# Performance work log

Hardware: AMD Instinct MI355X
Metric: run time of the kernel (lower is better)

## Reference

```python
import jax, jax.numpy as jnp
import numpy as np

N_NODES = 100000
N_EDGES = 1600000
IN_DIM = 128
HIDDEN = 128
OUT_DIM = 10
N_GRAPHS = 512
N_LAYERS = 3


def setup_inputs() -> dict:
    key = jax.random.key(0)
    ks = jax.random.split(key, 12)
    s_in = 1.0 / np.sqrt(IN_DIM)
    s_h = 1.0 / np.sqrt(HIDDEN)
    return {
        "x": jax.random.normal(ks[0], (N_NODES, IN_DIM), jnp.float32),
        "lin1_w": jax.random.normal(ks[1], (IN_DIM, HIDDEN), jnp.float32) * s_in,
        "lin1_b": jnp.zeros((HIDDEN,), jnp.float32),
        "gcn_w": jax.random.normal(ks[2], (N_LAYERS, HIDDEN, HIDDEN), jnp.float32) * s_h,
        "gcn_b": jnp.zeros((N_LAYERS, HIDDEN), jnp.float32),
        "lin_out_w": jax.random.normal(ks[3], (HIDDEN, HIDDEN), jnp.float32) * s_h,
        "lin_out_b": jnp.zeros((HIDDEN,), jnp.float32),
        "cls_w": jax.random.normal(ks[4], (HIDDEN, OUT_DIM), jnp.float32) * s_h,
        "cls_b": jnp.zeros((OUT_DIM,), jnp.float32),
        "edge_index": jax.random.randint(ks[5], (2, N_EDGES), 0, N_NODES, jnp.int64),
        "batch": jnp.sort(jax.random.randint(ks[6], (N_NODES,), 0, N_GRAPHS, jnp.int64)),
    }


def reference(x, lin1_w, lin1_b, gcn_w, gcn_b, lin_out_w, lin_out_b, cls_w, cls_b, edge_index, batch):
    n = x.shape[0]
    # GCNConv normalization with added self-loops (PyG default)
    row, col = edge_index[0], edge_index[1]
    loop = jnp.arange(n)
    row2 = jnp.concatenate([row, loop])  # source (message origin)
    col2 = jnp.concatenate([col, loop])  # target (aggregation index)
    deg = jax.ops.segment_sum(jnp.ones_like(col2, dtype=x.dtype), col2, num_segments=n)
    dinv = jax.lax.rsqrt(jnp.maximum(deg, 1.0))
    norm = (dinv[row2] * dinv[col2])[:, None]  # [E+N, 1]

    counts = jax.ops.segment_sum(jnp.ones((n,), x.dtype), batch, num_segments=N_GRAPHS)
    counts = jnp.maximum(counts, 1.0)[:, None]

    def readout_mean(h):  # global_mean_pool -> [G, H]
        return jax.ops.segment_sum(h, batch, num_segments=N_GRAPHS) / counts

    # lin1 + elu (dropout = identity in eval mode)
    h = jax.nn.elu(x @ lin1_w + lin1_b)
    reps = readout_mean(h)  # readout_layers[0]; l_sum accumulates layer reps
    for i in range(N_LAYERS):
        hw = h @ gcn_w[i]                       # [N, H]
        msg = norm * hw[row2]                   # gather + scale
        agg = jax.ops.segment_sum(msg, col2, num_segments=n)  # scatter-add
        h = jax.nn.elu(agg + gcn_b[i])          # GCNConv bias then NaOp act
        # pooling op is 'none' (remove_pooling=True): graph unchanged
        reps = reps + readout_mean(h)           # readout_layers[i+1], summed by LaOp 'l_sum'
    g = jax.nn.elu(reps @ lin_out_w + lin_out_b)
    logits = g @ cls_w + cls_b
    return jax.nn.log_softmax(logits, axis=-1)
```

## Files before the change

kernel.cpp:

```cpp
#include <hip/hip_runtime.h>
#include <hip/hip_bf16.h>
#include <math.h>

#define NN 100000
#define NE 1600000
#define HID 128
#define NG 512
#define NB 512
#define RB 196
#define CHUNK 4096
#define NPART ((NE + CHUNK - 1) / CHUNK)
#define GEMM_GRID ((NN + 127) / 128)

typedef unsigned short ushort_t;
typedef __attribute__((ext_vector_type(8))) short bf16x8;
typedef __attribute__((ext_vector_type(8))) unsigned short ushort8_t;
typedef __attribute__((ext_vector_type(4))) float f32x4;

__device__ __forceinline__ ushort_t f2bf(float v) {
    unsigned u = __float_as_uint(v);
    unsigned r = (u + 0x7FFF + ((u >> 16) & 1)) >> 16;
    return (ushort_t)r;
}
__device__ __forceinline__ float bf2f(ushort_t u) {
    return __uint_as_float((unsigned)u << 16);
}


__global__ __launch_bounds__(256) void hist_and_prepw(const int* __restrict__ ecol, int* __restrict__ ghist, int E,
                                                      const float* __restrict__ lin1_w,
                                                      const float* __restrict__ gcn_w,
                                                      ushort_t* __restrict__ wt_hi,
                                                      ushort_t* __restrict__ wt_lo) {
    if (blockIdx.x < 512) {
        __shared__ int lh[NB];
        for (int i = threadIdx.x; i < NB; i += 256) lh[i] = 0;
        __syncthreads();
        for (int e = blockIdx.x * 256 + threadIdx.x; e < E; e += 512 * 256)
            atomicAdd(&lh[ecol[e] / RB], 1);
        __syncthreads();
        for (int i = threadIdx.x; i < NB; i += 256) {
            int c = lh[i];
            if (c) atomicAdd(&ghist[i], c);
        }
    } else {
        int mb = blockIdx.x - 512;
        int m = mb >> 3;
        int chunk = mb & 7;
        const float* W = (m == 0) ? lin1_w : gcn_w + (size_t)(m - 1) * 16384;
        ushort_t* hi = wt_hi + (size_t)m * 16384;
        ushort_t* lo = wt_lo + (size_t)m * 16384;
        for (int i = chunk * 2048 + threadIdx.x; i < (chunk + 1) * 2048; i += 256) {
            int j = i & 7;
            int lane = (i >> 3) & 63;
            int ks = (i >> 9) & 3;
            int ct = (i >> 11) & 7;
            int n = ct * 16 + (lane & 15);
            int k = ks * 32 + (lane >> 4) * 8 + j;
            float v = W[k * 128 + n];
            ushort_t h = f2bf(v);
            hi[i] = h;
            lo[i] = f2bf(v - bf2f(h));
        }
    }
}

__global__ __launch_bounds__(NB) void bucket_scan(const int* __restrict__ ghist, int* __restrict__ brp,
                                                  int* __restrict__ gcur, int* __restrict__ rp,
                                                  const int* __restrict__ batch, float* __restrict__ invcnt) {
    __shared__ int s[NB];
    int t = threadIdx.x;
    int v = ghist[t];
    s[t] = v;
    __syncthreads();
    for (int off = 1; off < NB; off <<= 1) {
        int x = (t >= off) ? s[t - off] : 0;
        __syncthreads();
        s[t] += x;
        __syncthreads();
    }
    int ex = s[t] - v;
    brp[t] = ex;
    gcur[t] = ex;
    if (t == NB - 1) { brp[NB] = s[t]; rp[NN] = s[t]; }

    int lo = 0, hi = NN;
    while (lo < hi) { int m = (lo + hi) >> 1; if (batch[m] < t) lo = m + 1; else hi = m; }
    int s0 = lo;
    lo = 0; hi = NN;
    while (lo < hi) { int m = (lo + hi) >> 1; if (batch[m] < t + 1) lo = m + 1; else hi = m; }
    int c = lo - s0;
    invcnt[t] = 1.0f / (float)(c > 0 ? c : 1);
}

template<bool F32A, int MODE>
__device__ __forceinline__ void gemm_body(int bid, int tid,
                                          const float* __restrict__ A,
                                          const ushort_t* __restrict__ a_bf,
                                          const ushort_t* __restrict__ wt_hi,
                                          const ushort_t* __restrict__ wt_lo,
                                          const float* __restrict__ bias,
                                          const float* __restrict__ dinv,
                                          ushort_t* __restrict__ out0,
                                          int N) {
    const int lane = tid & 63;
    const int wid = tid >> 6;
    const int rowBase = bid * 128 + wid * 32;
    const int rblk = rowBase >> 4;
    const int l15 = lane & 15, lg = lane >> 4;

    f32x4 acc[2][8];
#pragma unroll
    for (int rt = 0; rt < 2; ++rt)
#pragma unroll
        for (int ct = 0; ct < 8; ++ct) acc[rt][ct] = (f32x4){0.f, 0.f, 0.f, 0.f};

#pragma unroll
    for (int ks = 0; ks < 4; ++ks) {
        bf16x8 ahi[2], alo[2];
#pragma unroll
        for (int rt = 0; rt < 2; ++rt) {
            int r = rowBase + rt * 16 + l15;
            if (F32A) {
                float av[8];
                if (r < N) {
                    const float* ap = A + (size_t)r * 128 + ks * 32 + lg * 8;
                    float4 a0 = *(const float4*)(ap);
                    float4 a1 = *(const float4*)(ap + 4);
                    av[0] = a0.x; av[1] = a0.y; av[2] = a0.z; av[3] = a0.w;
                    av[4] = a1.x; av[5] = a1.y; av[6] = a1.z; av[7] = a1.w;
                } else {
#pragma unroll
                    for (int j = 0; j < 8; ++j) av[j] = 0.f;
                }
#pragma unroll
                for (int j = 0; j < 8; ++j) {
                    ushort_t h = f2bf(av[j]);
                    ahi[rt][j] = (short)h;
                    alo[rt][j] = (short)f2bf(av[j] - bf2f(h));
                }
            } else {
                if (r < N) {
                    ahi[rt] = *(const bf16x8*)(a_bf + (size_t)(rblk + rt) * 2048 + (ks * 4 + lg) * 128 + l15 * 8);
                } else {
                    bf16x8 z = {0, 0, 0, 0, 0, 0, 0, 0};
                    ahi[rt] = z;
                }
            }
        }
#pragma unroll
        for (int ct = 0; ct < 8; ++ct) {
            size_t boff = (size_t)(((ct * 4 + ks) * 64 + lane) * 8);
            bf16x8 bhi = *(const bf16x8*)(wt_hi + boff);
            bf16x8 blo = *(const bf16x8*)(wt_lo + boff);
            acc[0][ct] = __builtin_amdgcn_mfma_f32_16x16x32_bf16(ahi[0], bhi, acc[0][ct], 0, 0, 0);
            acc[1][ct] = __builtin_amdgcn_mfma_f32_16x16x32_bf16(ahi[1], bhi, acc[1][ct], 0, 0, 0);
            acc[0][ct] = __builtin_amdgcn_mfma_f32_16x16x32_bf16(ahi[0], blo, acc[0][ct], 0, 0, 0);
            acc[1][ct] = __builtin_amdgcn_mfma_f32_16x16x32_bf16(ahi[1], blo, acc[1][ct], 0, 0, 0);
            if (F32A) {
                acc[0][ct] = __builtin_amdgcn_mfma_f32_16x16x32_bf16(alo[0], bhi, acc[0][ct], 0, 0, 0);
                acc[1][ct] = __builtin_amdgcn_mfma_f32_16x16x32_bf16(alo[1], bhi, acc[1][ct], 0, 0, 0);
            }
        }
    }

#pragma unroll
    for (int rt = 0; rt < 2; ++rt) {
#pragma unroll
        for (int reg = 0; reg < 4; ++reg) {
            int row = rowBase + rt * 16 + lg * 4 + reg;
            if (row >= N) continue;
            if (MODE == 0) {
                int r16 = lg * 4 + reg;
#pragma unroll
                for (int ct = 0; ct < 8; ++ct) {
                    int colc = ct * 16 + l15;
                    float v = acc[rt][ct][reg] + bias[colc];
                    v = v > 0.f ? v : expf(v) - 1.f;
                    out0[(size_t)(rblk + rt) * 2048 + (colc >> 3) * 128 + r16 * 8 + (colc & 7)] = f2bf(v);
                }
            } else {
                float dv = dinv[row];
#pragma unroll
                for (int ct = 0; ct < 8; ++ct) {
                    int colc = ct * 16 + l15;
                    out0[(size_t)row * 128 + colc] = f2bf(acc[rt][ct][reg] * dv);
                }
            }
        }
    }
}

__global__ __launch_bounds__(256) void part_gemm1(const int* __restrict__ erow, const int* __restrict__ ecol,
                                                  int* __restrict__ gcur, unsigned int* __restrict__ pairs, int E,
                                                  const float* __restrict__ x,
                                                  const ushort_t* __restrict__ wt_hi,
                                                  const ushort_t* __restrict__ wt_lo,
                                                  const float* __restrict__ lin1_b,
                                                  ushort_t* __restrict__ h) {
    if (blockIdx.x < NPART) {
        __shared__ int cnt[NB];
        __shared__ int base[NB];
        const int t = threadIdx.x;
        const int e0 = blockIdx.x * CHUNK;
        const int e1 = min(e0 + CHUNK, E);
        for (int i = t; i < NB; i += 256) cnt[i] = 0;
        __syncthreads();
        for (int e = e0 + t; e < e1; e += 256) atomicAdd(&cnt[ecol[e] / RB], 1);
        __syncthreads();
        for (int i = t; i < NB; i += 256) {
            int c = cnt[i];
            base[i] = c ? atomicAdd(&gcur[i], c) : 0;
            cnt[i] = 0;
        }
        __syncthreads();
        for (int e = e0 + t; e < e1; e += 256) {
            int d = ecol[e];
            int b = d / RB;
            int off = atomicAdd(&cnt[b], 1);
            pairs[base[b] + off] = ((unsigned)erow[e] << 8) | (unsigned)(d - b * RB);
        }
    } else {
        gemm_body<true, 0>(blockIdx.x - NPART, threadIdx.x, x, nullptr, wt_hi, wt_lo,
                           lin1_b, nullptr, h, NN);
    }
}

__global__ __launch_bounds__(256) void fill_readout0(const unsigned int* __restrict__ pairs, const int* __restrict__ brp,
                                                     int* __restrict__ rp, float* __restrict__ dinv,
                                                     int* __restrict__ csrc,
                                                     const ushort_t* __restrict__ h,
                                                     const int* __restrict__ batch,
                                                     const float* __restrict__ invcnt,
                                                     float* __restrict__ reps) {
    if (blockIdx.x < NB) {
        __shared__ int cnt[RB];
        __shared__ int cur[RB];
        __shared__ int sc[256];
        const int b = blockIdx.x, t = threadIdx.x;
        const int nbase = b * RB;
        const int s = brp[b], e = brp[b + 1];
        for (int i = t; i < RB; i += 256) cnt[i] = 0;
        __syncthreads();
        for (int i = s + t; i < e; i += 256) atomicAdd(&cnt[pairs[i] & 255u], 1);
        __syncthreads();
        int v = (t < RB) ? cnt[t] : 0;
        sc[t] = v;
        __syncthreads();
        for (int off = 1; off < 256; off <<= 1) {
            int x = (t >= off) ? sc[t - off] : 0;
            __syncthreads();
            sc[t] += x;
            __syncthreads();
        }
        if (t < RB) {
            int ex = s + sc[t] - v;
            int node = nbase + t;
            if (node < NN) {
                rp[node] = ex;
                dinv[node] = rsqrtf((float)v + 1.0f);
            }
            cur[t] = ex;
        }
        __syncthreads();
        for (int i = s + t; i < e; i += 256) {
            unsigned int p = pairs[i];
            int slot = atomicAdd(&cur[p & 255u], 1);
            csrc[slot] = (int)(p >> 8);
        }
    } else {
        int bb = blockIdx.x - NB;
        int g = bb >> 2;
        int part = bb & 3;
        int lo = 0, hi = NN;
        while (lo < hi) { int m = (lo + hi) >> 1; if (batch[m] < g) lo = m + 1; else hi = m; }
        int s = lo;
        lo = 0; hi = NN;
        while (lo < hi) { int m = (lo + hi) >> 1; if (batch[m] < g + 1) lo = m + 1; else hi = m; }
        int e = lo;

        __shared__ float sh[16][136];
        int ns = (int)(threadIdx.x >> 4);
        int L  = (int)(threadIdx.x & 15);
        int c8 = L << 3;
        float acc[8] = {};
        for (int v = s + part + ns * 4; v < e; v += 64) {
            ushort8_t t = *(const ushort8_t*)(h + (size_t)(v >> 4) * 2048 + L * 128 + (v & 15) * 8);
#pragma unroll
            for (int j = 0; j < 8; ++j) acc[j] += bf2f(t[j]);
        }
#pragma unroll
        for (int j = 0; j < 8; ++j) sh[ns][c8 + j] = acc[j];
        __syncthreads();
        if (threadIdx.x < 128) {
            int c = (int)threadIdx.x;
            float sum = 0.f;
#pragma unroll
            for (int k = 0; k < 16; ++k) sum += sh[k][c];
            unsafeAtomicAdd(&reps[(size_t)g * 128 + c], sum * invcnt[g]);
        }
    }
}

__global__ __launch_bounds__(256) void gemm_gcn(const ushort_t* __restrict__ a_bf,
                                                const ushort_t* __restrict__ wt_hi,
                                                const ushort_t* __restrict__ wt_lo,
                                                const float* __restrict__ dinv,
                                                ushort_t* __restrict__ hwb) {
    gemm_body<false, 1>(blockIdx.x, threadIdx.x, nullptr, a_bf, wt_hi, wt_lo,
                        nullptr, dinv, hwb, NN);
}

__global__ __launch_bounds__(256) void gather_agg(const int* __restrict__ rp,
                                                  const int* __restrict__ csrc,
                                                  const float* __restrict__ dinv,
                                                  const ushort_t* __restrict__ hwb,
                                                  const float* __restrict__ bias,
                                                  const int* __restrict__ batch,
                                                  const float* __restrict__ invcnt,
                                                  float* __restrict__ reps,
                                                  ushort_t* __restrict__ h_out) {
    __shared__ float sh[16][136];
    __shared__ int gid[16];
    const int v0 = blockIdx.x * 16;
    const int ns = (int)(threadIdx.x >> 4);
    int v = v0 + ns;
    int L = (int)(threadIdx.x & 15);
    int c8 = L << 3;
    if (threadIdx.x < 16) {
        int bidx = v0 + (int)threadIdx.x;
        if (bidx > NN - 1) bidx = NN - 1;
        gid[threadIdx.x] = batch[bidx];
    }

    float acc[8] = {};
    if (v < NN) {
        int s = rp[v], e = rp[v + 1];
        int i = s;
        for (; i + 16 <= e; i += 16) {
            int u[16];
#pragma unroll
            for (int k = 0; k < 16; ++k) u[k] = csrc[i + k];
            ushort8_t r[16];
#pragma unroll
            for (int k = 0; k < 16; ++k) r[k] = *(const ushort8_t*)(hwb + (size_t)u[k] * 128 + c8);
#pragma unroll
            for (int k = 0; k < 16; ++k)
#pragma unroll
                for (int j = 0; j < 8; ++j) acc[j] += bf2f(r[k][j]);
        }
        for (; i + 8 <= e; i += 8) {
            int u[8];
#pragma unroll
            for (int k = 0; k < 8; ++k) u[k] = csrc[i + k];
            ushort8_t r[8];
#pragma unroll
            for (int k = 0; k < 8; ++k) r[k] = *(const ushort8_t*)(hwb + (size_t)u[k] * 128 + c8);
#pragma unroll
            for (int k = 0; k < 8; ++k)
#pragma unroll
                for (int j = 0; j < 8; ++j) acc[j] += bf2f(r[k][j]);
        }
        for (; i < e; ++i) {
            int u = csrc[i];
            ushort8_t r0 = *(const ushort8_t*)(hwb + (size_t)u * 128 + c8);
#pragma unroll
            for (int j = 0; j < 8; ++j) acc[j] += bf2f(r0[j]);
        }

        float di = dinv[v];
        ushort8_t sv = *(const ushort8_t*)(hwb + (size_t)v * 128 + c8);
        ushort8_t o;
#pragma unroll
        for (int j = 0; j < 8; ++j) {
            float t = di * (acc[j] + bf2f(sv[j])) + bias[c8 + j];
            t = t > 0.f ? t : expf(t) - 1.f;
            acc[j] = t;
            o[j] = f2bf(t);
        }
        *(ushort8_t*)(h_out + (size_t)blockIdx.x * 2048 + L * 128 + ns * 8) = o;
    } else {
#pragma unroll
        for (int j = 0; j < 8; ++j) acc[j] = 0.f;
    }

#pragma unroll
    for (int j = 0; j < 8; ++j) sh[ns][c8 + j] = acc[j];
    __syncthreads();
    if (threadIdx.x < 128) {
        int c = (int)threadIdx.x;
        int nvalid = NN - v0;
        if (nvalid > 16) nvalid = 16;
        float run = sh[0][c];
        int cg = gid[0];
        for (int k = 1; k < nvalid; ++k) {
            int g2 = gid[k];
            if (g2 != cg) {
                unsafeAtomicAdd(&reps[(size_t)cg * 128 + c], run * invcnt[cg]);
                run = 0.f;
                cg = g2;
            }
            run += sh[k][c];
        }
        unsafeAtomicAdd(&reps[(size_t)cg * 128 + c], run * invcnt[cg]);
    }
}

__global__ __launch_bounds__(128) void head_fused(const float* __restrict__ reps,
                                                  const float* __restrict__ wout,
                                                  const float* __restrict__ bout,
                                                  const float* __restrict__ cw,
                                                  const float* __restrict__ cb,
                                                  float* __restrict__ out) {
    __shared__ float rrow[128];
    __shared__ float gg[128];
    __shared__ float lg[10];
    int t = threadIdx.x;
    int g = blockIdx.x;
    rrow[t] = reps[(size_t)g * 128 + t];
    __syncthreads();
    float a = bout[t];
    for (int k = 0; k < 128; ++k) a = fmaf(rrow[k], wout[k * 128 + t], a);
    a = a > 0.f ? a : expf(a) - 1.f;
    gg[t] = a;
    __syncthreads();
    if (t < 10) {
        float s = cb[t];
        for (int k = 0; k < 128; ++k) s = fmaf(gg[k], cw[k * 10 + t], s);
        lg[t] = s;
    }
    __syncthreads();
    if (t == 0) {
        float m = lg[0];
#pragma unroll
        for (int j = 1; j < 10; ++j) m = fmaxf(m, lg[j]);
        float se = 0.f;
#pragma unroll
        for (int j = 0; j < 10; ++j) se += expf(lg[j] - m);
        float L = logf(se);
#pragma unroll
        for (int j = 0; j < 10; ++j) out[(size_t)g * 10 + j] = lg[j] - m - L;
    }
}

extern "C" void kernel_launch(void* const* d_in, const int* in_sizes, int n_in,
                              void* d_out, int out_size, void* d_ws, size_t ws_size,
                              hipStream_t stream) {
    const float* x        = (const float*)d_in[0];
    const float* lin1_w   = (const float*)d_in[1];
    const float* lin1_b   = (const float*)d_in[2];
    const float* gcn_w    = (const float*)d_in[3];
    const float* gcn_b    = (const float*)d_in[4];
    const float* lin_out_w= (const float*)d_in[5];
    const float* lin_out_b= (const float*)d_in[6];
    const float* cls_w    = (const float*)d_in[7];
    const float* cls_b    = (const float*)d_in[8];
    const int*   ei       = (const int*)d_in[9];
    const int*   batch    = (const int*)d_in[10];
    float* out = (float*)d_out;

    const int* erow = ei;
    const int* ecol = ei + NE;

    ushort_t* h     = (ushort_t*)d_ws;
    ushort_t* hwb   = h + (size_t)NN * 128;
    float*    dinv  = (float*)(hwb + (size_t)NN * 128);
    float*    reps  = dinv + NN;
    float*    invcnt= reps + (size_t)NG * 128;
    int*      rp    = (int*)(invcnt + NG);
    int*      csrc  = rp + NN + 1;
    int*      ghist = csrc + NE;
    int*      brp   = ghist + NB;
    int*      gcur  = brp + NB + 1;
    ushort_t* wt_hi = (ushort_t*)(gcur + NB);
    ushort_t* wt_lo = wt_hi + 4 * 16384;
    unsigned int* pairs = (unsigned int*)(wt_lo + 4 * 16384);

    hipMemsetAsync(ghist, 0, NB * sizeof(int), stream);
    hipMemsetAsync(reps, 0, (size_t)NG * 128 * sizeof(float), stream);

    hist_and_prepw<<<512 + 32, 256, 0, stream>>>(ecol, ghist, NE, lin1_w, gcn_w, wt_hi, wt_lo);
    bucket_scan<<<1, NB, 0, stream>>>(ghist, brp, gcur, rp, batch, invcnt);
    part_gemm1<<<NPART + GEMM_GRID, 256, 0, stream>>>(erow, ecol, gcur, pairs, NE,
                                                      x, wt_hi, wt_lo, lin1_b, h);
    fill_readout0<<<NB + NG * 4, 256, 0, stream>>>(pairs, brp, rp, dinv, csrc,
                                                   h, batch, invcnt, reps);

    for (int i = 0; i < 3; ++i) {
        gemm_gcn<<<GEMM_GRID, 256, 0, stream>>>(h, wt_hi + (size_t)(i + 1) * 16384,
                                                wt_lo + (size_t)(i + 1) * 16384,
                                                dinv, hwb);
        gather_agg<<<(NN + 15) / 16, 256, 0, stream>>>(rp, csrc, dinv, hwb,
                                                       gcn_b + (size_t)i * 128,
                                                       batch, invcnt, reps, h);
    }

    head_fused<<<NG, 128, 0, stream>>>(reps, lin_out_w, lin_out_b, cls_w, cls_b, out);
}
```

Measured before the change: 434.2 us.

## Replace atomic bucket partition with per-block histograms and deterministic scanned offsets

The histogram kernel now writes per-chunk (16384 edges) bucket counts instead of atomically accumulating a global histogram. The scan kernel computes per-chunk base offsets for every bucket, so the partition pass no longer re-counts edges or does global atomicAdd on cursors. This removes one pass over ecol and the global atomic contention, and drops a memset. In exchange the partition uses fewer, larger blocks (98 instead of 391), and the single-block scan serially walks 98 chunks per bucket.

Result: no change. 427.1 us (-1.6%).

```diff
diff --git a/kernel.cpp b/kernel.cpp
--- a/kernel.cpp
+++ b/kernel.cpp
@@ -8,8 +8,8 @@
 #define NG 512
 #define NB 512
 #define RB 196
-#define CHUNK 4096
-#define NPART ((NE + CHUNK - 1) / CHUNK)
+#define PCHUNK 16384
+#define NPARTB ((NE + PCHUNK - 1) / PCHUNK)
 #define GEMM_GRID ((NN + 127) / 128)
 
 typedef unsigned short ushort_t;
@@ -27,24 +27,23 @@
 }
 
 
-__global__ __launch_bounds__(256) void hist_and_prepw(const int* __restrict__ ecol, int* __restrict__ ghist, int E,
-                                                      const float* __restrict__ lin1_w,
-                                                      const float* __restrict__ gcn_w,
-                                                      ushort_t* __restrict__ wt_hi,
-                                                      ushort_t* __restrict__ wt_lo) {
-    if (blockIdx.x < 512) {
+__global__ __launch_bounds__(256) void hist_prepw(const int* __restrict__ ecol, int* __restrict__ bcount,
+                                                  const float* __restrict__ lin1_w,
+                                                  const float* __restrict__ gcn_w,
+                                                  ushort_t* __restrict__ wt_hi,
+                                                  ushort_t* __restrict__ wt_lo) {
+    if (blockIdx.x < NPARTB) {
         __shared__ int lh[NB];
-        for (int i = threadIdx.x; i < NB; i += 256) lh[i] = 0;
-        __syncthreads();
-        for (int e = blockIdx.x * 256 + threadIdx.x; e < E; e += 512 * 256)
-            atomicAdd(&lh[ecol[e] / RB], 1);
-        __syncthreads();
-        for (int i = threadIdx.x; i < NB; i += 256) {
-            int c = lh[i];
-            if (c) atomicAdd(&ghist[i], c);
-        }
+        const int blk = blockIdx.x, t = threadIdx.x;
+        for (int i = t; i < NB; i += 256) lh[i] = 0;
+        __syncthreads();
+        const int e0 = blk * PCHUNK;
+        const int e1 = min(e0 + PCHUNK, NE);
+        for (int e = e0 + t; e < e1; e += 256) atomicAdd(&lh[ecol[e] / RB], 1);
+        __syncthreads();
+        for (int i = t; i < NB; i += 256) bcount[blk * NB + i] = lh[i];
     } else {
-        int mb = blockIdx.x - 512;
+        int mb = blockIdx.x - NPARTB;
         int m = mb >> 3;
         int chunk = mb & 7;
         const float* W = (m == 0) ? lin1_w : gcn_w + (size_t)(m - 1) * 16384;
@@ -65,13 +64,18 @@
     }
 }
 
-__global__ __launch_bounds__(NB) void bucket_scan(const int* __restrict__ ghist, int* __restrict__ brp,
-                                                  int* __restrict__ gcur, int* __restrict__ rp,
-                                                  const int* __restrict__ batch, float* __restrict__ invcnt) {
+__global__ __launch_bounds__(NB) void scan_bases(const int* __restrict__ bcount, int* __restrict__ basew,
+                                                 int* __restrict__ brp, int* __restrict__ rp,
+                                                 const int* __restrict__ batch, float* __restrict__ invcnt) {
     __shared__ int s[NB];
     int t = threadIdx.x;
-    int v = ghist[t];
-    s[t] = v;
+    int tot = 0;
+    for (int k = 0; k < NPARTB; ++k) {
+        int c = bcount[k * NB + t];
+        basew[k * NB + t] = tot;
+        tot += c;
+    }
+    s[t] = tot;
     __syncthreads();
     for (int off = 1; off < NB; off <<= 1) {
         int x = (t >= off) ? s[t - off] : 0;
@@ -79,9 +83,8 @@
         s[t] += x;
         __syncthreads();
     }
-    int ex = s[t] - v;
+    int ex = s[t] - tot;
     brp[t] = ex;
-    gcur[t] = ex;
     if (t == NB - 1) { brp[NB] = s[t]; rp[NN] = s[t]; }
 
     int lo = 0, hi = NN;
@@ -192,36 +195,32 @@
 }
 
 __global__ __launch_bounds__(256) void part_gemm1(const int* __restrict__ erow, const int* __restrict__ ecol,
-                                                  int* __restrict__ gcur, unsigned int* __restrict__ pairs, int E,
+                                                  const int* __restrict__ brp, const int* __restrict__ basew,
+                                                  unsigned int* __restrict__ pairs,
                                                   const float* __restrict__ x,
                                                   const ushort_t* __restrict__ wt_hi,
                                                   const ushort_t* __restrict__ wt_lo,
                                                   const float* __restrict__ lin1_b,
                                                   ushort_t* __restrict__ h) {
-    if (blockIdx.x < NPART) {
-        __shared__ int cnt[NB];
-        __shared__ int base[NB];
-        const int t = threadIdx.x;
-        const int e0 = blockIdx.x * CHUNK;
-        const int e1 = min(e0 + CHUNK, E);
-        for (int i = t; i < NB; i += 256) cnt[i] = 0;
-        __syncthreads();
-        for (int e = e0 + t; e < e1; e += 256) atomicAdd(&cnt[ecol[e] / RB], 1);
-        __syncthreads();
+    if (blockIdx.x < NPARTB) {
+        __shared__ int sbase[NB];
+        __shared__ int lcnt[NB];
+        const int blk = blockIdx.x, t = threadIdx.x;
         for (int i = t; i < NB; i += 256) {
-            int c = cnt[i];
-            base[i] = c ? atomicAdd(&gcur[i], c) : 0;
-            cnt[i] = 0;
-        }
-        __syncthreads();
+            sbase[i] = brp[i] + basew[blk * NB + i];
+            lcnt[i] = 0;
+        }
+        __syncthreads();
+        const int e0 = blk * PCHUNK;
+        const int e1 = min(e0 + PCHUNK, NE);
         for (int e = e0 + t; e < e1; e += 256) {
             int d = ecol[e];
             int b = d / RB;
-            int off = atomicAdd(&cnt[b], 1);
-            pairs[base[b] + off] = ((unsigned)erow[e] << 8) | (unsigned)(d - b * RB);
+            int off = atomicAdd(&lcnt[b], 1);
+            pairs[sbase[b] + off] = ((unsigned)erow[e] << 8) | (unsigned)(d - b * RB);
         }
     } else {
-        gemm_body<true, 0>(blockIdx.x - NPART, threadIdx.x, x, nullptr, wt_hi, wt_lo,
+        gemm_body<true, 0>(blockIdx.x - NPARTB, threadIdx.x, x, nullptr, wt_hi, wt_lo,
                            lin1_b, nullptr, h, NN);
     }
 }
@@ -469,20 +468,19 @@
     float*    invcnt= reps + (size_t)NG * 128;
     int*      rp    = (int*)(invcnt + NG);
     int*      csrc  = rp + NN + 1;
-    int*      ghist = csrc + NE;
-    int*      brp   = ghist + NB;
-    int*      gcur  = brp + NB + 1;
-    ushort_t* wt_hi = (ushort_t*)(gcur + NB);
+    int*      brp   = csrc + NE;
+    int*      bcount= brp + NB + 1;
+    int*      basew = bcount + NPARTB * NB;
+    ushort_t* wt_hi = (ushort_t*)(basew + NPARTB * NB);
     ushort_t* wt_lo = wt_hi + 4 * 16384;
     unsigned int* pairs = (unsigned int*)(wt_lo + 4 * 16384);
 
-    hipMemsetAsync(ghist, 0, NB * sizeof(int), stream);
     hipMemsetAsync(reps, 0, (size_t)NG * 128 * sizeof(float), stream);
 
-    hist_and_prepw<<<512 + 32, 256, 0, stream>>>(ecol, ghist, NE, lin1_w, gcn_w, wt_hi, wt_lo);
-    bucket_scan<<<1, NB, 0, stream>>>(ghist, brp, gcur, rp, batch, invcnt);
-    part_gemm1<<<NPART + GEMM_GRID, 256, 0, stream>>>(erow, ecol, gcur, pairs, NE,
-                                                      x, wt_hi, wt_lo, lin1_b, h);
+    hist_prepw<<<NPARTB + 32, 256, 0, stream>>>(ecol, bcount, lin1_w, gcn_w, wt_hi, wt_lo);
+    scan_bases<<<1, NB, 0, stream>>>(bcount, basew, brp, rp, batch, invcnt);
+    part_gemm1<<<NPARTB + GEMM_GRID, 256, 0, stream>>>(erow, ecol, brp, basew, pairs,
+                                                       x, wt_hi, wt_lo, lin1_b, h);
     fill_readout0<<<NB + NG * 4, 256, 0, stream>>>(pairs, brp, rp, dinv, csrc,
                                                    h, batch, invcnt, reps);
 
```
